# Kernel tuning notes

Hardware: AMD Instinct MI355X
Metric: run time of the kernel (lower is better)

## Reference

```python
import jax, jax.numpy as jnp
import numpy as np

ALPHA = 0.9
BETA = 0.85
THRESHOLD = 1.0
SIM_TIME = 128  # simulation_time
SURR_SCALE = 100.0


@jax.custom_vjp
def spike(x):
    # Heaviside step (SurrGradSpike.forward)
    return (x > 0).astype(x.dtype)

def _spike_fwd(x):
    return spike(x), x

def _spike_bwd(x, g):
    # fast-sigmoid surrogate gradient (Zenke & Ganguli 2018)
    return (g / (SURR_SCALE * jnp.abs(x) + 1.0) ** 2,)

spike.defvjp(_spike_fwd, _spike_bwd)


def setup_inputs() -> dict:
    key = jax.random.key(0)
    k0, k1, k2, k3 = jax.random.split(key, 4)
    B, IN, H = 16384, 128, 512
    inputs = jax.random.normal(k0, (B, IN), dtype=jnp.float32)
    # architecture[0] is doubled by the pos/neg input split -> W0: [2*IN, H]
    W0 = jax.random.normal(k1, (2 * IN, H), dtype=jnp.float32)
    W1 = jax.random.normal(k2, (H, H), dtype=jnp.float32)
    W2 = jax.random.normal(k3, (H, H), dtype=jnp.float32)
    return {"inputs": inputs, "W0": W0, "W1": W1, "W2": W2}


def _forward(inputs, Ws):
    # split input into positive / rectified-negative halves, concat on feature dim
    x = jnp.concatenate([jnp.maximum(inputs, 0.0), jnp.maximum(-inputs, 0.0)], axis=1)
    B = x.shape[0]
    L = len(Ws)
    syn0 = tuple(jnp.zeros((B, W.shape[1]), x.dtype) for W in Ws)
    mem0 = tuple(jnp.zeros((B, W.shape[1]), x.dtype) for W in Ws)

    def step(carry, _):
        syn, mem = carry
        new_syn, new_mem = [], []
        prev_spk = None
        for l, W in enumerate(Ws):
            h = jnp.einsum("bi,ij->bj", x if l == 0 else prev_spk, W)
            s = h if l == 0 else ALPHA * syn[l] + h  # layer 0: 0*syn + h
            m = BETA * mem[l] + s
            if l < L - 1:
                mthr = m - THRESHOLD
                prev_spk = spike(mthr)
                m = jnp.where(mthr > 0, 0.0, m)  # reset spiked membranes
            new_syn.append(s)
            new_mem.append(m)
        return (tuple(new_syn), tuple(new_mem)), None

    # t=0 in the original only records zeros and skips the update -> run T-1 steps
    (syn, mem), _ = jax.lax.scan(step, (syn0, mem0), None, length=SIM_TIME - 1)
    # returned value = mem_rec[-1][-1]: last layer membrane at final timestep
    return mem[-1]


def reference(inputs, W0, W1, W2):
    return _forward(inputs, (W0, W1, W2))
```

## Files before the change

kernel.cpp:

```cpp
#include <hip/hip_runtime.h>
#include <stdint.h>


typedef __attribute__((ext_vector_type(4))) float f32x4;

#define ALPHA 0.9f
#define BETA 0.85f
#define NSTEPS 127
#define WGT 1024
#define ROWS 32
#define CPAD 36
#define HPAD 516

#define LIF_L0(M, H, SP) { float _m = BETA * (M) + (H); \
    const bool _b = (_m - 1.0f) > 0.0f; (M) = _b ? 0.0f : _m; \
    (SP) = _b ? 1.0f : 0.0f; }
#define LIF_MID(S, M, A, SP) { (S) = ALPHA * (S) + (A); \
    float _m = BETA * (M) + (S); const bool _b = (_m - 1.0f) > 0.0f; \
    (M) = _b ? 0.0f : _m; (SP) = _b ? 1.0f : 0.0f; }
#define LIF_OUT(S, M, A) { (S) = ALPHA * (S) + (A); (M) = BETA * (M) + (S); }

__global__ __launch_bounds__(WGT, 4)
void dsnn_kernel(const float* __restrict__ x,
                 const float* __restrict__ W0,
                 const float* __restrict__ W1,
                 const float* __restrict__ W2,
                 float* __restrict__ out)
{
    __shared__ float spkbuf[512 * CPAD];
    __shared__ float h0buf[ROWS * HPAD];

    const int t  = threadIdx.x;
    const int c4 = (t & 127) * 4;
    const int g4 = (t >> 7) * 4;
    const int r0 = blockIdx.x * ROWS;

    for (int k = t; k < 256 * ROWS; k += WGT) {
        const int i = k >> 5;
        const int r = k & 31;
        const float v = (i < 128) ? x[(size_t)(r0 + r) * 128 + i]
                                  : -x[(size_t)(r0 + r) * 128 + (i - 128)];
        spkbuf[i * CPAD + r] = fmaxf(v, 0.0f);
    }
    __syncthreads();

    float acc[4][4];

    auto gemm = [&](const float* Wcol, int K) {
        #pragma unroll 4
        for (int j = 0; j < K; ++j) {
            const f32x4 s4 = *(const f32x4*)(spkbuf + j * CPAD + g4);
            const f32x4 wv = *(const f32x4*)(Wcol + (size_t)j * 512);
            #pragma unroll
            for (int r = 0; r < 4; ++r) {
                acc[r][0] = fmaf(s4[r], wv.x, acc[r][0]);
                acc[r][1] = fmaf(s4[r], wv.y, acc[r][1]);
                acc[r][2] = fmaf(s4[r], wv.z, acc[r][2]);
                acc[r][3] = fmaf(s4[r], wv.w, acc[r][3]);
            }
        }
    };

    #pragma unroll
    for (int r = 0; r < 4; ++r)
        #pragma unroll
        for (int cc = 0; cc < 4; ++cc) acc[r][cc] = 0.0f;
    gemm(W0 + c4, 256);
    #pragma unroll
    for (int r = 0; r < 4; ++r) {
        f32x4 hv = { acc[r][0], acc[r][1], acc[r][2], acc[r][3] };
        *(f32x4*)(h0buf + (g4 + r) * HPAD + c4) = hv;
    }
    __syncthreads();

    float m0[4][4], s1[4][4], m1[4][4], s2[4][4], m2[4][4];
    #pragma unroll
    for (int r = 0; r < 4; ++r)
        #pragma unroll
        for (int cc = 0; cc < 4; ++cc) {
            m0[r][cc] = 0.f; s1[r][cc] = 0.f; m1[r][cc] = 0.f;
            s2[r][cc] = 0.f; m2[r][cc] = 0.f;
        }

    float sarr[4][4];

    for (int step = 0; step < NSTEPS; ++step) {
        #pragma unroll
        for (int r = 0; r < 4; ++r) {
            const f32x4 hv = *(const f32x4*)(h0buf + (g4 + r) * HPAD + c4);
            LIF_L0(m0[r][0], hv.x, sarr[0][r]);
            LIF_L0(m0[r][1], hv.y, sarr[1][r]);
            LIF_L0(m0[r][2], hv.z, sarr[2][r]);
            LIF_L0(m0[r][3], hv.w, sarr[3][r]);
        }
        #pragma unroll
        for (int cc = 0; cc < 4; ++cc) {
            f32x4 sv = { sarr[cc][0], sarr[cc][1], sarr[cc][2], sarr[cc][3] };
            *(f32x4*)(spkbuf + (c4 + cc) * CPAD + g4) = sv;
        }
        __syncthreads();

        #pragma unroll
        for (int r = 0; r < 4; ++r)
            #pragma unroll
            for (int cc = 0; cc < 4; ++cc) acc[r][cc] = 0.0f;
        gemm(W1 + c4, 512);
        __syncthreads();

        #pragma unroll
        for (int r = 0; r < 4; ++r) {
            LIF_MID(s1[r][0], m1[r][0], acc[r][0], sarr[0][r]);
            LIF_MID(s1[r][1], m1[r][1], acc[r][1], sarr[1][r]);
            LIF_MID(s1[r][2], m1[r][2], acc[r][2], sarr[2][r]);
            LIF_MID(s1[r][3], m1[r][3], acc[r][3], sarr[3][r]);
        }
        #pragma unroll
        for (int cc = 0; cc < 4; ++cc) {
            f32x4 sv = { sarr[cc][0], sarr[cc][1], sarr[cc][2], sarr[cc][3] };
            *(f32x4*)(spkbuf + (c4 + cc) * CPAD + g4) = sv;
        }
        __syncthreads();

        #pragma unroll
        for (int r = 0; r < 4; ++r)
            #pragma unroll
            for (int cc = 0; cc < 4; ++cc) acc[r][cc] = 0.0f;
        gemm(W2 + c4, 512);
        #pragma unroll
        for (int r = 0; r < 4; ++r) {
            LIF_OUT(s2[r][0], m2[r][0], acc[r][0]);
            LIF_OUT(s2[r][1], m2[r][1], acc[r][1]);
            LIF_OUT(s2[r][2], m2[r][2], acc[r][2]);
            LIF_OUT(s2[r][3], m2[r][3], acc[r][3]);
        }
        __syncthreads();
    }

    #pragma unroll
    for (int r = 0; r < 4; ++r) {
        f32x4 ov = { m2[r][0], m2[r][1], m2[r][2], m2[r][3] };
        *(f32x4*)(out + (size_t)(r0 + g4 + r) * 512 + c4) = ov;
    }
}

extern "C" void kernel_launch(void* const* d_in, const int* in_sizes, int n_in,
                              void* d_out, int out_size, void* d_ws, size_t ws_size,
                              hipStream_t stream) {
    const float* inputs = (const float*)d_in[0];
    const float* W0     = (const float*)d_in[1];
    const float* W1     = (const float*)d_in[2];
    const float* W2     = (const float*)d_in[3];
    float* out          = (float*)d_out;

    dim3 grid(16384 / ROWS);
    dim3 block(WGT);
    dsnn_kernel<<<grid, block, 0, stream>>>(inputs, W0, W1, W2, out);
}
```

Baseline: 33.39 ms.

## Reshape per-thread tile to 16 rows by 2 columns with 512-thread blocks

Each thread now computes a 16x2 output tile instead of 4x4, and the workgroup shrinks to 512 threads. This halves the number of global weight load instructions per block while spike values are read as wave-uniform broadcasts from shared memory. In exchange, per-thread register state roughly doubles and occupancy changes, which could reduce latency hiding.

```diff
diff --git a/kernel.cpp b/kernel.cpp
--- a/kernel.cpp
+++ b/kernel.cpp
@@ -2,12 +2,13 @@
 #include <stdint.h>
 
 
+typedef __attribute__((ext_vector_type(2))) float f32x2;
 typedef __attribute__((ext_vector_type(4))) float f32x4;
 
 #define ALPHA 0.9f
 #define BETA 0.85f
 #define NSTEPS 127
-#define WGT 1024
+#define WGT 512
 #define ROWS 32
 #define CPAD 36
 #define HPAD 516
@@ -20,7 +21,7 @@
     (M) = _b ? 0.0f : _m; (SP) = _b ? 1.0f : 0.0f; }
 #define LIF_OUT(S, M, A) { (S) = ALPHA * (S) + (A); (M) = BETA * (M) + (S); }
 
-__global__ __launch_bounds__(WGT, 4)
+__global__ __launch_bounds__(WGT, 2)
 void dsnn_kernel(const float* __restrict__ x,
                  const float* __restrict__ W0,
                  const float* __restrict__ W1,
@@ -31,8 +32,8 @@
     __shared__ float h0buf[ROWS * HPAD];
 
     const int t  = threadIdx.x;
-    const int c4 = (t & 127) * 4;
-    const int g4 = (t >> 7) * 4;
+    const int c2 = (t & 255) * 2;
+    const int g  = (t >> 8) * 16;
     const int r0 = blockIdx.x * ROWS;
 
     for (int k = t; k < 256 * ROWS; k += WGT) {
@@ -44,102 +45,100 @@
     }
     __syncthreads();
 
-    float acc[4][4];
+    float acc[16][2];
 
     auto gemm = [&](const float* Wcol, int K) {
         #pragma unroll 4
         for (int j = 0; j < K; ++j) {
-            const f32x4 s4 = *(const f32x4*)(spkbuf + j * CPAD + g4);
-            const f32x4 wv = *(const f32x4*)(Wcol + (size_t)j * 512);
+            const float* sb = spkbuf + j * CPAD + g;
+            const f32x4 sA = *(const f32x4*)(sb);
+            const f32x4 sB = *(const f32x4*)(sb + 4);
+            const f32x4 sC = *(const f32x4*)(sb + 8);
+            const f32x4 sD = *(const f32x4*)(sb + 12);
+            const f32x2 wv = *(const f32x2*)(Wcol + (size_t)j * 512);
             #pragma unroll
-            for (int r = 0; r < 4; ++r) {
-                acc[r][0] = fmaf(s4[r], wv.x, acc[r][0]);
-                acc[r][1] = fmaf(s4[r], wv.y, acc[r][1]);
-                acc[r][2] = fmaf(s4[r], wv.z, acc[r][2]);
-                acc[r][3] = fmaf(s4[r], wv.w, acc[r][3]);
+            for (int rr = 0; rr < 4; ++rr) {
+                acc[rr][0]      = fmaf(sA[rr], wv.x, acc[rr][0]);
+                acc[rr][1]      = fmaf(sA[rr], wv.y, acc[rr][1]);
+                acc[4 + rr][0]  = fmaf(sB[rr], wv.x, acc[4 + rr][0]);
+                acc[4 + rr][1]  = fmaf(sB[rr], wv.y, acc[4 + rr][1]);
+                acc[8 + rr][0]  = fmaf(sC[rr], wv.x, acc[8 + rr][0]);
+                acc[8 + rr][1]  = fmaf(sC[rr], wv.y, acc[8 + rr][1]);
+                acc[12 + rr][0] = fmaf(sD[rr], wv.x, acc[12 + rr][0]);
+                acc[12 + rr][1] = fmaf(sD[rr], wv.y, acc[12 + rr][1]);
             }
         }
     };
 
     #pragma unroll
-    for (int r = 0; r < 4; ++r)
-        #pragma unroll
-        for (int cc = 0; cc < 4; ++cc) acc[r][cc] = 0.0f;
-    gemm(W0 + c4, 256);
+    for (int r = 0; r < 16; ++r) { acc[r][0] = 0.0f; acc[r][1] = 0.0f; }
+    gemm(W0 + c2, 256);
     #pragma unroll
-    for (int r = 0; r < 4; ++r) {
-        f32x4 hv = { acc[r][0], acc[r][1], acc[r][2], acc[r][3] };
-        *(f32x4*)(h0buf + (g4 + r) * HPAD + c4) = hv;
+    for (int r = 0; r < 16; ++r) {
+        f32x2 hv = { acc[r][0], acc[r][1] };
+        *(f32x2*)(h0buf + (g + r) * HPAD + c2) = hv;
     }
     __syncthreads();
 
-    float m0[4][4], s1[4][4], m1[4][4], s2[4][4], m2[4][4];
+    float m0[16][2], s1[16][2], m1[16][2], s2[16][2], m2[16][2];
     #pragma unroll
-    for (int r = 0; r < 4; ++r)
+    for (int r = 0; r < 16; ++r)
         #pragma unroll
-        for (int cc = 0; cc < 4; ++cc) {
+        for (int cc = 0; cc < 2; ++cc) {
             m0[r][cc] = 0.f; s1[r][cc] = 0.f; m1[r][cc] = 0.f;
             s2[r][cc] = 0.f; m2[r][cc] = 0.f;
         }
 
-    float sarr[4][4];
-
     for (int step = 0; step < NSTEPS; ++step) {
         #pragma unroll
-        for (int r = 0; r < 4; ++r) {
-            const f32x4 hv = *(const f32x4*)(h0buf + (g4 + r) * HPAD + c4);
-            LIF_L0(m0[r][0], hv.x, sarr[0][r]);
-            LIF_L0(m0[r][1], hv.y, sarr[1][r]);
-            LIF_L0(m0[r][2], hv.z, sarr[2][r]);
-            LIF_L0(m0[r][3], hv.w, sarr[3][r]);
-        }
-        #pragma unroll
-        for (int cc = 0; cc < 4; ++cc) {
-            f32x4 sv = { sarr[cc][0], sarr[cc][1], sarr[cc][2], sarr[cc][3] };
-            *(f32x4*)(spkbuf + (c4 + cc) * CPAD + g4) = sv;
+        for (int rg = 0; rg < 4; ++rg) {
+            f32x4 sv0, sv1;
+            #pragma unroll
+            for (int rr = 0; rr < 4; ++rr) {
+                const int r = rg * 4 + rr;
+                const f32x2 hv = *(const f32x2*)(h0buf + (g + r) * HPAD + c2);
+                LIF_L0(m0[r][0], hv.x, sv0[rr]);
+                LIF_L0(m0[r][1], hv.y, sv1[rr]);
+            }
+            *(f32x4*)(spkbuf + c2 * CPAD + g + rg * 4)       = sv0;
+            *(f32x4*)(spkbuf + (c2 + 1) * CPAD + g + rg * 4) = sv1;
         }
         __syncthreads();
 
         #pragma unroll
-        for (int r = 0; r < 4; ++r)
-            #pragma unroll
-            for (int cc = 0; cc < 4; ++cc) acc[r][cc] = 0.0f;
-        gemm(W1 + c4, 512);
+        for (int r = 0; r < 16; ++r) { acc[r][0] = 0.0f; acc[r][1] = 0.0f; }
+        gemm(W1 + c2, 512);
         __syncthreads();
 
         #pragma unroll
-        for (int r = 0; r < 4; ++r) {
-            LIF_MID(s1[r][0], m1[r][0], acc[r][0], sarr[0][r]);
-            LIF_MID(s1[r][1], m1[r][1], acc[r][1], sarr[1][r]);
-            LIF_MID(s1[r][2], m1[r][2], acc[r][2], sarr[2][r]);
-            LIF_MID(s1[r][3], m1[r][3], acc[r][3], sarr[3][r]);
-        }
-        #pragma unroll
-        for (int cc = 0; cc < 4; ++cc) {
-            f32x4 sv = { sarr[cc][0], sarr[cc][1], sarr[cc][2], sarr[cc][3] };
-            *(f32x4*)(spkbuf + (c4 + cc) * CPAD + g4) = sv;
+        for (int rg = 0; rg < 4; ++rg) {
+            f32x4 sv0, sv1;
+            #pragma unroll
+            for (int rr = 0; rr < 4; ++rr) {
+                const int r = rg * 4 + rr;
+                LIF_MID(s1[r][0], m1[r][0], acc[r][0], sv0[rr]);
+                LIF_MID(s1[r][1], m1[r][1], acc[r][1], sv1[rr]);
+            }
+            *(f32x4*)(spkbuf + c2 * CPAD + g + rg * 4)       = sv0;
+            *(f32x4*)(spkbuf + (c2 + 1) * CPAD + g + rg * 4) = sv1;
         }
         __syncthreads();
 
         #pragma unroll
-        for (int r = 0; r < 4; ++r)
-            #pragma unroll
-            for (int cc = 0; cc < 4; ++cc) acc[r][cc] = 0.0f;
-        gemm(W2 + c4, 512);
+        for (int r = 0; r < 16; ++r) { acc[r][0] = 0.0f; acc[r][1] = 0.0f; }
+        gemm(W2 + c2, 512);
         #pragma unroll
-        for (int r = 0; r < 4; ++r) {
+        for (int r = 0; r < 16; ++r) {
             LIF_OUT(s2[r][0], m2[r][0], acc[r][0]);
             LIF_OUT(s2[r][1], m2[r][1], acc[r][1]);
-            LIF_OUT(s2[r][2], m2[r][2], acc[r][2]);
-            LIF_OUT(s2[r][3], m2[r][3], acc[r][3]);
         }
         __syncthreads();
     }
 
     #pragma unroll
-    for (int r = 0; r < 4; ++r) {
-        f32x4 ov = { m2[r][0], m2[r][1], m2[r][2], m2[r][3] };
-        *(f32x4*)(out + (size_t)(r0 + g4 + r) * 512 + c4) = ov;
+    for (int r = 0; r < 16; ++r) {
+        f32x2 ov = { m2[r][0], m2[r][1] };
+        *(f32x2*)(out + (size_t)(r0 + g + r) * 512 + c2) = ov;
     }
 }
 
```

Result: slower. 40.93 ms (+22.6%).
